# Kernel optimization log

Measured on AMD Instinct MI355X. Metric: run time of the kernel, lower is better.

## Reference

```python
import jax, jax.numpy as jnp
import numpy as np

K_MAX, K_MIN = 12.0, 1.0
TEMP = 1.0
STE_ALPHA = 12.0
EPS = 1e-8

DIM, HID, KHID, WHID = 512, 2048, 128, 128
B, N = 8, 1024


def setup_inputs() -> dict:
    key = jax.random.key(0)
    ks = jax.random.split(key, 13)
    def lin(k, fan_in, shape):
        bound = 1.0 / np.sqrt(fan_in)
        return jax.random.uniform(k, shape, jnp.float32, -bound, bound)
    return {
        "x": jax.random.normal(ks[0], (B, N, DIM), jnp.float32),
        "fc1_w": lin(ks[1], DIM, (HID, DIM)),
        "fc1_b": lin(ks[2], DIM, (HID,)),
        "fc2_w": lin(ks[3], HID, (DIM, HID)),
        "fc2_b": lin(ks[4], HID, (DIM,)),
        "k1_w": lin(ks[5], DIM, (KHID, DIM)),
        "k1_b": lin(ks[6], DIM, (KHID,)),
        "k2_w": lin(ks[7], KHID, (3, KHID)),
        "k2_b": lin(ks[8], KHID, (3,)),
        "w1_w": lin(ks[9], DIM, (WHID, DIM)),
        "w1_b": lin(ks[10], DIM, (WHID,)),
        "w2_w": lin(ks[11], WHID, (3, WHID)),
        "w2_b": lin(ks[12], WHID, (3,)),
    }


def adaptive_knn_aggregate(h, k_cont):
    # h: (B,N,C), k_cont: (B,) continuous k in [k_min, k_max]
    sim = jnp.einsum("bnc,bmc->bnm", h, h) / TEMP          # (B,N,N)
    order = jnp.argsort(-sim, axis=-1)                      # descending
    rank = jnp.argsort(order, axis=-1).astype(h.dtype)      # rank 0 = most similar
    # soft top-k gate (STE-style sigmoid around k_cont)
    gate = jax.nn.sigmoid(STE_ALPHA * (k_cont[:, None, None] - (rank + 0.5)))
    attn = jax.nn.softmax(sim, axis=-1) * gate
    attn = attn / (attn.sum(axis=-1, keepdims=True) + EPS)
    return jnp.einsum("bnm,bmc->bnc", attn, h)


def reference(x, fc1_w, fc1_b, fc2_w, fc2_b, k1_w, k1_b, k2_w, k2_b,
              w1_w, w1_b, w2_w, w2_b):
    pooled = x.mean(axis=1)                                 # (B,C)
    # adaptive k values net
    kh = jax.nn.relu(pooled @ k1_w.T + k1_b)
    ratio = jax.nn.sigmoid(kh @ k2_w.T + k2_b)              # (B,3)
    k_cont = K_MIN + ratio * (K_MAX - K_MIN)
    # adaptive branch weights net
    wh = jax.nn.relu(pooled @ w1_w.T + w1_b)
    w = jax.nn.softmax(wh @ w2_w.T + w2_b, axis=-1)         # (B,3)
    # MLP (dropout p=0 -> identity)
    h = jax.nn.relu(x @ fc1_w.T + fc1_b)
    h = h @ fc2_w.T + fc2_b                                 # (B,N,C)
    # three KNN aggregation branches blended by w
    y = sum(adaptive_knn_aggregate(h, k_cont[:, i]) * w[:, i, None, None]
            for i in range(3))
    return y
```

## Files before the change

kernel.cpp:

```cpp
#include <hip/hip_runtime.h>
#include <math.h>

#define DIM_ 512
#define HID_ 2048
#define B_ 8
#define N_ 1024
#define ROWS_ 8192
#define TOPK 16

typedef __attribute__((ext_vector_type(8))) short short8;
typedef __attribute__((ext_vector_type(16))) float float16v;
typedef __attribute__((ext_vector_type(4))) float float4v;

__device__ __forceinline__ float sigm(float x) { return 1.f / (1.f + __expf(-x)); }

__device__ __forceinline__ short f2bf(float f) {
    unsigned u = __float_as_uint(f);
    u += 0x7FFF + ((u >> 16) & 1);
    return (short)(u >> 16);
}

__device__ __forceinline__ float bf2f(unsigned short s) {
    return __uint_as_float((unsigned)s << 16);
}

__device__ __forceinline__ unsigned f2ord(float f) {
    unsigned u = __float_as_uint(f);
    return (u & 0x80000000u) ? ~u : (u | 0x80000000u);
}

__device__ __forceinline__ void gload16(const short* g, short* l) {
    __builtin_amdgcn_global_load_lds(
        (const __attribute__((address_space(1))) void*)g,
        (__attribute__((address_space(3))) void*)l, 16, 0, 0);
}

__global__ __launch_bounds__(512)
void prep_kernel(const float* __restrict__ x, float* __restrict__ part, short* __restrict__ xb,
                 const float* __restrict__ w1, const float* __restrict__ w2,
                 short* __restrict__ o1, short* __restrict__ o2) {
    const int bx = blockIdx.x;
    if (bx < 256) {
        const int b = bx >> 5, chunk = bx & 31;
        const int c = threadIdx.x;
        const long long base = ((long long)b * N_ + chunk * 32) * DIM_ + c;
        const float* xp = x + base;
        short* xo = xb + base;
        float s = 0.f;
        for (int n = 0; n < 32; ++n) {
            const float v = xp[(long long)n * DIM_];
            s += v;
            xo[(long long)n * DIM_] = f2bf(v);
        }
        part[(long long)bx * DIM_ + c] = s;
    } else {
        const int n4 = HID_ * DIM_ / 4;
        int i = (bx - 256) * 2048 + threadIdx.x;
#pragma unroll
        for (int t = 0; t < 4; ++t, i += 512) {
            const float* in = (i < n4) ? w1 : w2;
            short* out = (i < n4) ? o1 : o2;
            const int j = (i < n4) ? i : (i - n4);
            const float4 v = *(const float4*)(in + (long long)j * 4);
            short4 o;
            o.x = f2bf(v.x); o.y = f2bf(v.y); o.z = f2bf(v.z); o.w = f2bf(v.w);
            *(short4*)(out + (long long)j * 4) = o;
        }
    }
}

__global__ __launch_bounds__(512)
void pool_heads_kernel(const float* __restrict__ part,
                       const float* __restrict__ k1w, const float* __restrict__ k1b,
                       const float* __restrict__ k2w, const float* __restrict__ k2b,
                       const float* __restrict__ w1w, const float* __restrict__ w1b,
                       const float* __restrict__ w2w, const float* __restrict__ w2b,
                       float* __restrict__ kcont, float* __restrict__ wbr) {
    const int b = blockIdx.x;
    const int t = threadIdx.x;
    __shared__ float sp[DIM_];
    __shared__ float kh[128], wh[128];
    __shared__ float wraw[4];
    float s = 0.f;
    for (int g = 0; g < 32; ++g) s += part[((long long)b * 32 + g) * DIM_ + t];
    sp[t] = s * (1.f / 1024.f);
    __syncthreads();
    if (t < 128) {
        float ak = k1b[t], aw = w1b[t];
        for (int k = 0; k < DIM_; ++k) {
            const float pv = sp[k];
            ak = fmaf(pv, k1w[t * DIM_ + k], ak);
            aw = fmaf(pv, w1w[t * DIM_ + k], aw);
        }
        kh[t] = fmaxf(ak, 0.f);
        wh[t] = fmaxf(aw, 0.f);
    }
    __syncthreads();
    if (t < 3) {
        float rk = k2b[t], rw = w2b[t];
        for (int k = 0; k < 128; ++k) {
            rk = fmaf(kh[k], k2w[t * 128 + k], rk);
            rw = fmaf(wh[k], w2w[t * 128 + k], rw);
        }
        kcont[b * 3 + t] = 1.f + 11.f * sigm(rk);
        wraw[t] = rw;
    }
    __syncthreads();
    if (t == 0) {
        const float m = fmaxf(wraw[0], fmaxf(wraw[1], wraw[2]));
        const float e0 = __expf(wraw[0] - m), e1 = __expf(wraw[1] - m), e2 = __expf(wraw[2] - m);
        const float inv = 1.f / (e0 + e1 + e2);
        wbr[b * 3 + 0] = e0 * inv;
        wbr[b * 3 + 1] = e1 * inv;
        wbr[b * 3 + 2] = e2 * inv;
    }
}

template<int OUTMODE, int BN, int SWZ>
__global__ __launch_bounds__(256)
void gemm_mfma(const short* __restrict__ A, const short* __restrict__ Bm,
               const float* __restrict__ bias,
               float* __restrict__ outF, short* __restrict__ outB,
               int M, int N, int K, int lda, int ldb,
               long long sA, long long sB, long long sC) {
    constexpr int NJ = BN / 64;
    int bz, mi, ni;
    if (SWZ == 1) {
        const int id = blockIdx.x + gridDim.x * (blockIdx.y + gridDim.y * blockIdx.z);
        bz = id % gridDim.z;
        const int r = id / gridDim.z;
        ni = r % gridDim.x;
        mi = r / gridDim.x;
    } else {
        const int id = blockIdx.x + gridDim.x * blockIdx.y;
        const int numM = gridDim.y;
        const int mg = numM >> 3;
        bz = blockIdx.z;
        mi = (id & 7) * mg + (id >> 3) % mg;
        ni = id / numM;
    }
    A  += (long long)bz * sA;
    Bm += (long long)bz * sB;

    __shared__ short As[128 * 64];
    __shared__ short Bs[BN * 64];

    const int tid = threadIdx.x;
    const int lane = tid & 63;
    const int wv = tid >> 6;
    const int m0 = mi * 128;
    const int n0 = ni * BN;

    const int lrow = lane >> 3;
    const int cg = (lane & 7) ^ lrow;

    const int ml = (wv & 1) * 64;
    const int nl = (wv >> 1) * (BN / 2);
    const int fr = lane & 31;
    const int khh = lane >> 5;

    float16v acc[2][NJ];
#pragma unroll
    for (int i = 0; i < 2; ++i)
#pragma unroll
        for (int j = 0; j < NJ; ++j)
#pragma unroll
            for (int r = 0; r < 16; ++r) acc[i][j][r] = 0.f;

    for (int k0 = 0; k0 < K; k0 += 64) {
        __syncthreads();
#pragma unroll
        for (int i = 0; i < 4; ++i) {
            const int rloc = wv * 32 + i * 8 + lrow;
            gload16(A + (long long)(m0 + rloc) * lda + (k0 + cg * 8),
                    &As[(wv * 32 + i * 8) * 64]);
        }
#pragma unroll
        for (int i = 0; i < BN / 32; ++i) {
            const int rloc = wv * (BN / 4) + i * 8 + lrow;
            gload16(Bm + (long long)(n0 + rloc) * ldb + (k0 + cg * 8),
                    &Bs[(wv * (BN / 4) + i * 8) * 64]);
        }
        __syncthreads();
#pragma unroll
        for (int c = 0; c < 4; ++c) {
            const int ch = c * 2 + khh;
            short8 af[2], bfr[NJ];
#pragma unroll
            for (int i = 0; i < 2; ++i) {
                const int m = ml + i * 32 + fr;
                af[i] = *(const short8*)&As[m * 64 + ((ch ^ (m & 7)) * 8)];
            }
#pragma unroll
            for (int j = 0; j < NJ; ++j) {
                const int n = nl + j * 32 + fr;
                bfr[j] = *(const short8*)&Bs[n * 64 + ((ch ^ (n & 7)) * 8)];
            }
#pragma unroll
            for (int i = 0; i < 2; ++i)
#pragma unroll
                for (int j = 0; j < NJ; ++j)
                    acc[i][j] = __builtin_amdgcn_mfma_f32_32x32x16_bf16(
                        af[i], bfr[j], acc[i][j], 0, 0, 0);
        }
    }

    const long long outOfs = (long long)bz * sC;
#pragma unroll
    for (int i = 0; i < 2; ++i) {
#pragma unroll
        for (int j = 0; j < NJ; ++j) {
            const int ng = n0 + nl + j * 32 + fr;
            float bv = 0.f;
            if (OUTMODE != 2) bv = bias[ng];
#pragma unroll
            for (int r = 0; r < 16; ++r) {
                const int mg2 = m0 + ml + i * 32 + (r & 3) + 8 * (r >> 2) + 4 * khh;
                float v = acc[i][j][r] + bv;
                if (OUTMODE == 0) v = fmaxf(v, 0.f);
                const long long idx = outOfs + (long long)mg2 * N + ng;
                if (OUTMODE == 2) outF[idx] = v;
                else              outB[idx] = f2bf(v);
            }
        }
    }
}

template<int OUTMODE, bool BATCH>
__global__ __launch_bounds__(512, 2)
void gemm256(const short* __restrict__ A, const short* __restrict__ Bm,
             const float* __restrict__ bias, float* __restrict__ outF,
             short* __restrict__ outB, int M, int N, int K, int lda, int ldb,
             int mTiles, long long sA, long long sB, long long sC) {
    __shared__ short As[2][256 * 64];
    __shared__ short Bs[2][256 * 64];

    const int tid = threadIdx.x;
    const int lane = tid & 63;
    const int wv = tid >> 6;
    const int l15 = lane & 15;
    const int kq = lane >> 4;
    const int lr = lane >> 3;
    const int cg = (lane & 7) ^ lr;

    const int id = blockIdx.x;
    const int xcd = id & 7;
    const int r = id >> 3;
    int mi, ni;
    const short* Ag = A;
    const short* Bg = Bm;
    long long cOfs = 0;
    if (BATCH) {
        mi = r % mTiles; ni = r / mTiles;
        Ag += (long long)xcd * sA; Bg += (long long)xcd * sB; cOfs = (long long)xcd * sC;
    } else {
        const int mg = mTiles >> 3;
        mi = xcd * mg + r % mg; ni = r / mg;
    }
    const int m0 = mi * 256, n0 = ni * 256;
    const int wm = wv >> 2, wn = wv & 3;

    float4v acc[8][4];
#pragma unroll
    for (int i = 0; i < 8; ++i)
#pragma unroll
        for (int j = 0; j < 4; ++j)
#pragma unroll
            for (int q = 0; q < 4; ++q) acc[i][j][q] = 0.f;

    const int sB1 = (wv & 3) + (wv >> 2) * 8;

    auto stA = [&](int bf, int s, int k0) {
        gload16(Ag + (long long)(m0 + s * 8 + lr) * lda + (k0 + cg * 8), &As[bf][s * 8 * 64]);
    };
    auto stB = [&](int bf, int s, int k0) {
        gload16(Bg + (long long)(n0 + s * 8 + lr) * ldb + (k0 + cg * 8), &Bs[bf][s * 8 * 64]);
    };
    auto unit0 = [&](int bf, int k0) {
        stA(bf, wv, k0); stA(bf, 16 + wv, k0);
        stB(bf, sB1, k0); stB(bf, 16 + sB1, k0);
    };
    auto unit1 = [&](int bf, int k0) { stA(bf, 8 + wv, k0); stA(bf, 24 + wv, k0); };
    auto unit2 = [&](int bf, int k0) { stB(bf, 4 + sB1, k0); stB(bf, 20 + sB1, k0); };

    auto tile_body = [&](int bf, int k1, bool stage) {
#pragma unroll
        for (int p = 0; p < 4; ++p) {
            const int mq = p & 1, nq = p >> 1;
            short8 af[4][2], bfr[2][2];
#pragma unroll
            for (int f = 0; f < 4; ++f) {
                const int rA = wm * 128 + mq * 64 + f * 16 + l15;
                const int ro = rA * 64, sw = rA & 7;
#pragma unroll
                for (int ks = 0; ks < 2; ++ks)
                    af[f][ks] = *(const short8*)&As[bf][ro + (((ks * 4 + kq) ^ sw) * 8)];
            }
#pragma unroll
            for (int g = 0; g < 2; ++g) {
                const int rB = wn * 64 + nq * 32 + g * 16 + l15;
                const int ro = rB * 64, sw = rB & 7;
#pragma unroll
                for (int ks = 0; ks < 2; ++ks)
                    bfr[g][ks] = *(const short8*)&Bs[bf][ro + (((ks * 4 + kq) ^ sw) * 8)];
            }
            if (stage) {
                if (p == 0) unit0(bf ^ 1, k1);
                else if (p == 1) unit1(bf ^ 1, k1);
                else if (p == 2) unit2(bf ^ 1, k1);
                if (p == 0 || p == 1) asm volatile("s_waitcnt vmcnt(6)" ::: "memory");
                else if (p == 3)      asm volatile("s_waitcnt vmcnt(4)" ::: "memory");
            } else {
                if (p == 0)      asm volatile("s_waitcnt vmcnt(2)" ::: "memory");
                else if (p == 1) asm volatile("s_waitcnt vmcnt(0)" ::: "memory");
            }
            __builtin_amdgcn_s_barrier();
            asm volatile("s_waitcnt lgkmcnt(0)" ::: "memory");
            __builtin_amdgcn_sched_barrier(0);
            __builtin_amdgcn_s_setprio(1);
#pragma unroll
            for (int f = 0; f < 4; ++f)
#pragma unroll
                for (int g = 0; g < 2; ++g)
#pragma unroll
                    for (int ks = 0; ks < 2; ++ks)
                        acc[mq * 4 + f][nq * 2 + g] = __builtin_amdgcn_mfma_f32_16x16x32_bf16(
                            af[f][ks], bfr[g][ks], acc[mq * 4 + f][nq * 2 + g], 0, 0, 0);
            __builtin_amdgcn_s_setprio(0);
            if (stage || p < 3) __builtin_amdgcn_s_barrier();
        }
    };

    const int NT = K >> 6;
    unit0(0, 0);
    __builtin_amdgcn_sched_barrier(0);
    unit1(0, 0);
    __builtin_amdgcn_sched_barrier(0);
    unit2(0, 0);
    asm volatile("s_waitcnt vmcnt(4)" ::: "memory");
    __builtin_amdgcn_s_barrier();

    for (int t = 0; t < NT - 1; ++t)
        tile_body(t & 1, (t + 1) << 6, true);
    tile_body((NT - 1) & 1, 0, false);

#pragma unroll
    for (int mf = 0; mf < 8; ++mf) {
#pragma unroll
        for (int nf = 0; nf < 4; ++nf) {
            const int ng = n0 + wn * 64 + nf * 16 + l15;
            float bv = 0.f;
            if (OUTMODE != 2) bv = bias[ng];
            const int mb = m0 + wm * 128 + mf * 16 + kq * 4;
#pragma unroll
            for (int q = 0; q < 4; ++q) {
                float v = acc[mf][nf][q] + bv;
                if (OUTMODE == 0) v = fmaxf(v, 0.f);
                const long long idx = cOfs + (long long)(mb + q) * N + ng;
                if (OUTMODE == 2) outF[idx] = v;
                else              outB[idx] = f2bf(v);
            }
        }
    }
}

__global__ __launch_bounds__(256)
void topk_agg_kernel(const float* __restrict__ sim,
                     const float* __restrict__ kcont, const float* __restrict__ wbr,
                     const unsigned short* __restrict__ h, float* __restrict__ y) {
    const int wv = threadIdx.x >> 6;
    const int lane = threadIdx.x & 63;
    const int ll = lane & 15;
    const int id = blockIdx.x;
    const int b = id & 7;
    const int row0 = b * N_ + (id >> 3) * 8 + wv * 2;
    const float* srowA = sim + (long long)row0 * N_;
    const float* srowB = srowA + N_;

    const int base = lane * 16;
    float fA[16], fB[16];
#pragma unroll
    for (int q = 0; q < 4; ++q) {
        const float4 va = *(const float4*)(srowA + base + q * 4);
        const float4 vb = *(const float4*)(srowB + base + q * 4);
        fA[q * 4 + 0] = va.x; fA[q * 4 + 1] = va.y; fA[q * 4 + 2] = va.z; fA[q * 4 + 3] = va.w;
        fB[q * 4 + 0] = vb.x; fB[q * 4 + 1] = vb.y; fB[q * 4 + 2] = vb.z; fB[q * 4 + 3] = vb.w;
    }

    float mA = fA[0], mB = fB[0];
#pragma unroll
    for (int j = 1; j < 16; ++j) { mA = fmaxf(mA, fA[j]); mB = fmaxf(mB, fB[j]); }
#pragma unroll
    for (int d = 32; d > 0; d >>= 1) {
        mA = fmaxf(mA, __shfl_xor(mA, d));
        mB = fmaxf(mB, __shfl_xor(mB, d));
    }
    const float maxvA = mA, maxvB = mB;

    float sAo = 0.f, sBo = 0.f;
#pragma unroll
    for (int j = 0; j < 16; ++j) { sAo += __expf(fA[j] - maxvA); sBo += __expf(fB[j] - maxvB); }
#pragma unroll
    for (int d = 32; d > 0; d >>= 1) {
        sAo += __shfl_xor(sAo, d);
        sBo += __shfl_xor(sBo, d);
    }
    const float invdenA = 1.f / sAo, invdenB = 1.f / sBo;

    unsigned keyA[16], keyB[16];
#pragma unroll
    for (int j = 0; j < 16; ++j) {
        keyA[j] = (f2ord(fA[j]) & 0xFFFFFC00u) | (unsigned)(1023 - (base + j));
        keyB[j] = (f2ord(fB[j]) & 0xFFFFFC00u) | (unsigned)(1023 - (base + j));
    }

#pragma unroll
    for (int k = 2; k <= 16; k <<= 1) {
#pragma unroll
        for (int j = k >> 1; j > 0; j >>= 1) {
#pragma unroll
            for (int i = 0; i < 16; ++i) {
                const int l = i ^ j;
                if (l > i) {
                    const bool desc = ((i & k) == 0);
                    {
                        const unsigned a = keyA[i], bk = keyA[l];
                        const unsigned hi = (a > bk) ? a : bk;
                        const unsigned lo = (a > bk) ? bk : a;
                        keyA[i] = desc ? hi : lo;
                        keyA[l] = desc ? lo : hi;
                    }
                    {
                        const unsigned a = keyB[i], bk = keyB[l];
                        const unsigned hi = (a > bk) ? a : bk;
                        const unsigned lo = (a > bk) ? bk : a;
                        keyB[i] = desc ? hi : lo;
                        keyB[l] = desc ? lo : hi;
                    }
                }
            }
        }
    }

#pragma unroll
    for (int d = 1; d < 64; d <<= 1) {
        unsigned oA[16], oB[16];
#pragma unroll
        for (int i = 0; i < 16; ++i) {
            oA[i] = __shfl_xor(keyA[15 - i], d);
            oB[i] = __shfl_xor(keyB[15 - i], d);
        }
#pragma unroll
        for (int i = 0; i < 16; ++i) {
            keyA[i] = (keyA[i] > oA[i]) ? keyA[i] : oA[i];
            keyB[i] = (keyB[i] > oB[i]) ? keyB[i] : oB[i];
        }
#pragma unroll
        for (int j = 8; j > 0; j >>= 1) {
#pragma unroll
            for (int i = 0; i < 16; ++i) {
                if ((i & j) == 0) {
                    {
                        const unsigned a = keyA[i], bk = keyA[i | j];
                        keyA[i]     = (a > bk) ? a : bk;
                        keyA[i | j] = (a > bk) ? bk : a;
                    }
                    {
                        const unsigned a = keyB[i], bk = keyB[i | j];
                        keyB[i]     = (a > bk) ? a : bk;
                        keyB[i | j] = (a > bk) ? bk : a;
                    }
                }
            }
        }
    }

    const int rowSel = (lane >> 4) & 1;
    unsigned k32 = 0;
#pragma unroll
    for (int j = 0; j < 16; ++j) {
        const unsigned sel = rowSel ? keyB[j] : keyA[j];
        k32 = (ll == j) ? sel : k32;
    }
    const int myidx = 1023 - (int)(k32 & 1023u);
    const float* srow = rowSel ? srowB : srowA;
    const float myval = srow[myidx];

    unsigned long long kx = ((unsigned long long)f2ord(myval) << 32)
                          | (unsigned)(1023 - myidx);
#pragma unroll
    for (int k = 2; k <= 16; k <<= 1) {
#pragma unroll
        for (int d = k >> 1; d > 0; d >>= 1) {
            const unsigned long long other = __shfl_xor(kx, d);
            const bool keepMax = (((ll & k) != 0) == ((ll & d) != 0));
            const bool mineBig = (kx > other);
            kx = (keepMax == mineBig) ? kx : other;
        }
    }
    const unsigned sord = (unsigned)(kx >> 32);
    const unsigned su = (sord & 0x80000000u) ? (sord & 0x7FFFFFFFu) : ~sord;
    const float sval = __uint_as_float(su);
    const int sidx = 1023 - (int)(kx & 1023u);

    const float kc0 = kcont[b * 3 + 0], kc1 = kcont[b * 3 + 1], kc2 = kcont[b * 3 + 2];
    const float w0 = wbr[b * 3 + 0], w1 = wbr[b * 3 + 1], w2 = wbr[b * 3 + 2];

    const float mv = rowSel ? maxvB : maxvA;
    const float ivd = rowSel ? invdenB : invdenA;
    const float p = __expf(sval - mv) * ivd;
    const float rr = (float)ll + 0.5f;
    const float g0 = sigm(12.f * (kc0 - rr));
    const float g1 = sigm(12.f * (kc1 - rr));
    const float g2 = sigm(12.f * (kc2 - rr));
    float s0 = p * g0, s1 = p * g1, s2 = p * g2;
#pragma unroll
    for (int d = 1; d < 16; d <<= 1) {
        s0 += __shfl_xor(s0, d);
        s1 += __shfl_xor(s1, d);
        s2 += __shfl_xor(s2, d);
    }
    const float f0 = w0 / (s0 + 1e-8f);
    const float f1 = w1 / (s1 + 1e-8f);
    const float f2 = w2 / (s2 + 1e-8f);
    const float mycoef = p * (f0 * g0 + f1 * g1 + f2 * g2);

    const unsigned short* hbase = h + (long long)b * (N_ * DIM_) + lane * 8;
    float accA[8] = {0.f, 0.f, 0.f, 0.f, 0.f, 0.f, 0.f, 0.f};
    float accB[8] = {0.f, 0.f, 0.f, 0.f, 0.f, 0.f, 0.f, 0.f};
    const int half = lane & 32;
#pragma unroll
    for (int r = 0; r < 16; ++r) {
        const float cA = __shfl(mycoef, half | r);
        const int   iA = __shfl(sidx,  half | r);
        const float cB = __shfl(mycoef, half | 16 | r);
        const int   iB = __shfl(sidx,  half | 16 | r);
        const ushort4 a0 = *(const ushort4*)(hbase + (long long)iA * DIM_);
        const ushort4 a1 = *(const ushort4*)(hbase + (long long)iA * DIM_ + 4);
        const ushort4 b0 = *(const ushort4*)(hbase + (long long)iB * DIM_);
        const ushort4 b1 = *(const ushort4*)(hbase + (long long)iB * DIM_ + 4);
        accA[0] = fmaf(cA, bf2f(a0.x), accA[0]);
        accA[1] = fmaf(cA, bf2f(a0.y), accA[1]);
        accA[2] = fmaf(cA, bf2f(a0.z), accA[2]);
        accA[3] = fmaf(cA, bf2f(a0.w), accA[3]);
        accA[4] = fmaf(cA, bf2f(a1.x), accA[4]);
        accA[5] = fmaf(cA, bf2f(a1.y), accA[5]);
        accA[6] = fmaf(cA, bf2f(a1.z), accA[6]);
        accA[7] = fmaf(cA, bf2f(a1.w), accA[7]);
        accB[0] = fmaf(cB, bf2f(b0.x), accB[0]);
        accB[1] = fmaf(cB, bf2f(b0.y), accB[1]);
        accB[2] = fmaf(cB, bf2f(b0.z), accB[2]);
        accB[3] = fmaf(cB, bf2f(b0.w), accB[3]);
        accB[4] = fmaf(cB, bf2f(b1.x), accB[4]);
        accB[5] = fmaf(cB, bf2f(b1.y), accB[5]);
        accB[6] = fmaf(cB, bf2f(b1.z), accB[6]);
        accB[7] = fmaf(cB, bf2f(b1.w), accB[7]);
    }
    float* ypA = y + (long long)row0 * DIM_ + lane * 8;
    float* ypB = ypA + DIM_;
    *(float4*)(ypA + 0) = make_float4(accA[0], accA[1], accA[2], accA[3]);
    *(float4*)(ypA + 4) = make_float4(accA[4], accA[5], accA[6], accA[7]);
    *(float4*)(ypB + 0) = make_float4(accB[0], accB[1], accB[2], accB[3]);
    *(float4*)(ypB + 4) = make_float4(accB[4], accB[5], accB[6], accB[7]);
}

extern "C" void kernel_launch(void* const* d_in, const int* in_sizes, int n_in,
                              void* d_out, int out_size, void* d_ws, size_t ws_size,
                              hipStream_t stream) {
    const float* x     = (const float*)d_in[0];
    const float* fc1_w = (const float*)d_in[1];
    const float* fc1_b = (const float*)d_in[2];
    const float* fc2_w = (const float*)d_in[3];
    const float* fc2_b = (const float*)d_in[4];
    const float* k1_w  = (const float*)d_in[5];
    const float* k1_b  = (const float*)d_in[6];
    const float* k2_w  = (const float*)d_in[7];
    const float* k2_b  = (const float*)d_in[8];
    const float* w1_w  = (const float*)d_in[9];
    const float* w1_b  = (const float*)d_in[10];
    const float* w2_w  = (const float*)d_in[11];
    const float* w2_b  = (const float*)d_in[12];

    char* ws = (char*)d_ws;
    short* h1b    = (short*)(ws + 0);
    float* simbuf = (float*)(ws + 0);
    short* xb     = (short*)(ws + 33554432);
    short* hb     = (short*)(ws + 67108864);
    short* w1b    = (short*)(ws + 75497472);
    short* w2b    = (short*)(ws + 77594624);
    float* ppart  = (float*)(ws + 79691776);
    float* kcont  = (float*)(ws + 80216064);
    float* wbr    = (float*)(ws + 80216192);

    float* y = (float*)d_out;

    prep_kernel<<<dim3(512), dim3(512), 0, stream>>>(x, ppart, xb, fc1_w, fc2_w, w1b, w2b);
    pool_heads_kernel<<<dim3(B_), dim3(512), 0, stream>>>(ppart, k1_w, k1_b, k2_w, k2_b,
                                                          w1_w, w1_b, w2_w, w2_b, kcont, wbr);
    gemm256<0, false><<<dim3(256), dim3(512), 0, stream>>>(
        xb, w1b, fc1_b, nullptr, h1b, ROWS_, HID_, DIM_, DIM_, DIM_, 32, 0, 0, 0);
    gemm_mfma<1, 64, 2><<<dim3(DIM_ / 64, ROWS_ / 128, 1), dim3(256), 0, stream>>>(
        h1b, w2b, fc2_b, nullptr, hb, ROWS_, DIM_, HID_, HID_, HID_, 0, 0, 0);
    gemm256<2, true><<<dim3(128), dim3(512), 0, stream>>>(
        hb, hb, nullptr, simbuf, nullptr, N_, N_, DIM_, DIM_, DIM_, 4,
        (long long)N_ * DIM_, (long long)N_ * DIM_, (long long)N_ * N_);
    topk_agg_kernel<<<dim3(ROWS_ / 8), dim3(256), 0, stream>>>(
        simbuf, kcont, wbr, (const unsigned short*)hb, y);
}
```

Before: 219.4 us.

## Vectorize x prep, parallelize pooled head matvecs, switch sim GEMM kernel

The x conversion and pooling pass now uses float4 loads and short4 stores, with each block split into 4 row groups. That produces 128 partial sums per batch instead of 32, and the kcont/wbr workspace offsets move to make room. The pooled-head matvec is now spread over all 8 waves with coalesced float4 weight reads and a shuffle reduction, replacing 128 threads that each walked a strided row serially. The batched similarity GEMM switches from the persistent gemm256 kernel to a 3D-grid gemm_mfma with 128-wide tiles, which changes occupancy and tiling for that stage.

Measured after the change: 212.1 us. 3.3% less time.

```diff
diff --git a/kernel.cpp b/kernel.cpp
--- a/kernel.cpp
+++ b/kernel.cpp
@@ -42,17 +42,21 @@
     const int bx = blockIdx.x;
     if (bx < 256) {
         const int b = bx >> 5, chunk = bx & 31;
-        const int c = threadIdx.x;
-        const long long base = ((long long)b * N_ + chunk * 32) * DIM_ + c;
-        const float* xp = x + base;
-        short* xo = xb + base;
-        float s = 0.f;
-        for (int n = 0; n < 32; ++n) {
-            const float v = xp[(long long)n * DIM_];
-            s += v;
-            xo[(long long)n * DIM_] = f2bf(v);
-        }
-        part[(long long)bx * DIM_ + c] = s;
+        const int cg = (threadIdx.x & 127) * 4;
+        const int rg = threadIdx.x >> 7;
+        const long long rbase = (long long)b * N_ + chunk * 32 + rg * 8;
+        const float* xp = x + rbase * DIM_ + cg;
+        short* xo = xb + rbase * DIM_ + cg;
+        float4 s = make_float4(0.f, 0.f, 0.f, 0.f);
+#pragma unroll
+        for (int n = 0; n < 8; ++n) {
+            const float4 v = *(const float4*)(xp + (long long)n * DIM_);
+            s.x += v.x; s.y += v.y; s.z += v.z; s.w += v.w;
+            short4 o;
+            o.x = f2bf(v.x); o.y = f2bf(v.y); o.z = f2bf(v.z); o.w = f2bf(v.w);
+            *(short4*)(xo + (long long)n * DIM_) = o;
+        }
+        *(float4*)(part + ((long long)bx * 4 + rg) * DIM_ + cg) = s;
     } else {
         const int n4 = HID_ * DIM_ / 4;
         int i = (bx - 256) * 2048 + threadIdx.x;
@@ -82,18 +86,42 @@
     __shared__ float kh[128], wh[128];
     __shared__ float wraw[4];
     float s = 0.f;
-    for (int g = 0; g < 32; ++g) s += part[((long long)b * 32 + g) * DIM_ + t];
+    for (int g = 0; g < 128; ++g) s += part[((long long)b * 128 + g) * DIM_ + t];
     sp[t] = s * (1.f / 1024.f);
     __syncthreads();
-    if (t < 128) {
-        float ak = k1b[t], aw = w1b[t];
-        for (int k = 0; k < DIM_; ++k) {
-            const float pv = sp[k];
-            ak = fmaf(pv, k1w[t * DIM_ + k], ak);
-            aw = fmaf(pv, w1w[t * DIM_ + k], aw);
-        }
-        kh[t] = fmaxf(ak, 0.f);
-        wh[t] = fmaxf(aw, 0.f);
+
+    const int wv = t >> 6, l = t & 63;
+    float sv[8];
+    {
+        const float4 a = *(const float4*)&sp[l * 8];
+        const float4 c = *(const float4*)&sp[l * 8 + 4];
+        sv[0] = a.x; sv[1] = a.y; sv[2] = a.z; sv[3] = a.w;
+        sv[4] = c.x; sv[5] = c.y; sv[6] = c.z; sv[7] = c.w;
+    }
+#pragma unroll 4
+    for (int i = 0; i < 16; ++i) {
+        const int r = wv * 16 + i;
+        const float4 k0 = *(const float4*)(k1w + (long long)r * DIM_ + l * 8);
+        const float4 k1 = *(const float4*)(k1w + (long long)r * DIM_ + l * 8 + 4);
+        const float4 q0 = *(const float4*)(w1w + (long long)r * DIM_ + l * 8);
+        const float4 q1 = *(const float4*)(w1w + (long long)r * DIM_ + l * 8 + 4);
+        float ak = sv[0] * k0.x;
+        ak = fmaf(sv[1], k0.y, ak); ak = fmaf(sv[2], k0.z, ak); ak = fmaf(sv[3], k0.w, ak);
+        ak = fmaf(sv[4], k1.x, ak); ak = fmaf(sv[5], k1.y, ak);
+        ak = fmaf(sv[6], k1.z, ak); ak = fmaf(sv[7], k1.w, ak);
+        float aw = sv[0] * q0.x;
+        aw = fmaf(sv[1], q0.y, aw); aw = fmaf(sv[2], q0.z, aw); aw = fmaf(sv[3], q0.w, aw);
+        aw = fmaf(sv[4], q1.x, aw); aw = fmaf(sv[5], q1.y, aw);
+        aw = fmaf(sv[6], q1.z, aw); aw = fmaf(sv[7], q1.w, aw);
+#pragma unroll
+        for (int d = 32; d > 0; d >>= 1) {
+            ak += __shfl_xor(ak, d);
+            aw += __shfl_xor(aw, d);
+        }
+        if (l == 0) {
+            kh[r] = fmaxf(ak + k1b[r], 0.f);
+            wh[r] = fmaxf(aw + w1b[r], 0.f);
+        }
     }
     __syncthreads();
     if (t < 3) {
@@ -589,8 +617,8 @@
     short* w1b    = (short*)(ws + 75497472);
     short* w2b    = (short*)(ws + 77594624);
     float* ppart  = (float*)(ws + 79691776);
-    float* kcont  = (float*)(ws + 80216064);
-    float* wbr    = (float*)(ws + 80216192);
+    float* kcont  = (float*)(ws + 81788928);
+    float* wbr    = (float*)(ws + 81789056);
 
     float* y = (float*)d_out;
 
@@ -601,8 +629,8 @@
         xb, w1b, fc1_b, nullptr, h1b, ROWS_, HID_, DIM_, DIM_, DIM_, 32, 0, 0, 0);
     gemm_mfma<1, 64, 2><<<dim3(DIM_ / 64, ROWS_ / 128, 1), dim3(256), 0, stream>>>(
         h1b, w2b, fc2_b, nullptr, hb, ROWS_, DIM_, HID_, HID_, HID_, 0, 0, 0);
-    gemm256<2, true><<<dim3(128), dim3(512), 0, stream>>>(
-        hb, hb, nullptr, simbuf, nullptr, N_, N_, DIM_, DIM_, DIM_, 4,
+    gemm_mfma<2, 128, 1><<<dim3(N_ / 128, N_ / 128, B_), dim3(256), 0, stream>>>(
+        hb, hb, nullptr, simbuf, nullptr, N_, N_, DIM_, DIM_, DIM_,
         (long long)N_ * DIM_, (long long)N_ * DIM_, (long long)N_ * N_);
     topk_agg_kernel<<<dim3(ROWS_ / 8), dim3(256), 0, stream>>>(
         simbuf, kcont, wbr, (const unsigned short*)hb, y);
```
